# Performance work log

Measured on AMD Instinct MI355X. Metric: run time of the kernel, lower is better.

## Reference

```python
import jax, jax.numpy as jnp
import numpy as np

N_EMBD = 768
N_HEADS = 12

def setup_inputs() -> dict:
    key = jax.random.key(0)
    ks = jax.random.split(key, 5)
    B, T, C = 8, 1024, N_EMBD
    s_in = 1.0 / np.sqrt(C)
    x = jax.random.normal(ks[0], (B, T, C), dtype=jnp.float32)
    W_attn = jax.random.normal(ks[1], (C, 3 * C), dtype=jnp.float32) * s_in
    b_attn = jnp.zeros((3 * C,), dtype=jnp.float32)
    W_proj = jax.random.normal(ks[2], (C, C), dtype=jnp.float32) * s_in
    b_proj = jnp.zeros((C,), dtype=jnp.float32)
    return {"x": x, "W_attn": W_attn, "b_attn": b_attn, "W_proj": W_proj, "b_proj": b_proj}

def reference(x, W_attn, b_attn, W_proj, b_proj):
    B, T, C = x.shape
    H = N_HEADS
    hd = C // H
    qkv = x @ W_attn + b_attn                      # [B,T,3C]
    q, k, v = jnp.split(qkv, 3, axis=-1)
    # [B,T,C] -> [B,H,T,hd]
    q = q.reshape(B, T, H, hd).transpose(0, 2, 1, 3)
    k = k.reshape(B, T, H, hd).transpose(0, 2, 1, 3)
    v = v.reshape(B, T, H, hd).transpose(0, 2, 1, 3)
    att = jnp.einsum('bhqd,bhkd->bhqk', q, k) * (1.0 / np.sqrt(hd))
    mask = jnp.tril(jnp.ones((T, T), dtype=bool))
    att = jnp.where(mask, att, -jnp.inf)
    att = jax.nn.softmax(att, axis=-1)
    y = jnp.einsum('bhqk,bhkd->bhqd', att, v)      # [B,H,T,hd]
    y = y.transpose(0, 2, 1, 3).reshape(B, T, C)
    return y @ W_proj + b_proj
```

## Files before the change

### kernel.cpp

```cpp
#include <hip/hip_runtime.h>
#include <hip/hip_bf16.h>
#include <cmath>

typedef __bf16 bf16_t;
typedef __bf16 bf16x8 __attribute__((ext_vector_type(8)));
typedef float f32x4 __attribute__((ext_vector_type(4)));

#define MFMA16(A, B, C) __builtin_amdgcn_mfma_f32_16x16x32_bf16(A, B, C, 0, 0, 0)

#define GLOAD_LDS16(g, l)                                                      \
  __builtin_amdgcn_global_load_lds(                                            \
      (const __attribute__((address_space(1))) void*)(g),                      \
      (__attribute__((address_space(3))) void*)(l), 16, 0, 0)

__global__ __launch_bounds__(256) void f32_to_bf16(
    const float* __restrict__ src, bf16_t* __restrict__ dst) {
  const size_t i = (size_t)blockIdx.x * 256 + threadIdx.x;
  const float4 a0 = ((const float4*)src)[i * 2];
  const float4 a1 = ((const float4*)src)[i * 2 + 1];
  bf16x8 v = {(bf16_t)a0.x, (bf16_t)a0.y, (bf16_t)a0.z, (bf16_t)a0.w,
              (bf16_t)a1.x, (bf16_t)a1.y, (bf16_t)a1.z, (bf16_t)a1.w};
  ((bf16x8*)dst)[i] = v;
}

__global__ __launch_bounds__(256) void transpose_f32_to_bf16(
    const float* __restrict__ src, bf16_t* __restrict__ dst, int R, int C) {
  __shared__ bf16_t tile[32][33];
  const int c0 = blockIdx.x * 32, r0 = blockIdx.y * 32;
  const int tr = threadIdx.x >> 5;
  const int tc = threadIdx.x & 31;
#pragma unroll
  for (int i = 0; i < 32; i += 8)
    tile[tr + i][tc] = (bf16_t)src[(size_t)(r0 + tr + i) * C + (c0 + tc)];
  __syncthreads();
#pragma unroll
  for (int i = 0; i < 32; i += 8)
    dst[(size_t)(c0 + tr + i) * R + (r0 + tc)] = tile[tc][tr + i];
}

__global__ __launch_bounds__(768, 1) void gemm_qkv(
    const bf16_t* __restrict__ A, const bf16_t* __restrict__ BT,
    const float* __restrict__ bias,
    bf16_t* __restrict__ o0, bf16_t* __restrict__ o1, bf16_t* __restrict__ o2,
    int K) {
  extern __shared__ __align__(16) bf16_t smem[];
  constexpr int ASZ = 256 * 64;
  constexpr int BSZ = 288 * 64;
  bf16_t* Bbase = smem + 2 * ASZ;

  const int tid = threadIdx.x;
  const int w = tid >> 6, lane = tid & 63;
  const int wr = w / 6, wc = w % 6;
  const int quad = lane >> 4, l16 = lane & 15;

  const int id = blockIdx.x;
  const int xcd = id & 7;
  const int lin = id >> 3;
  const int nt = lin & 7;
  const int mt = (xcd << 2) + (lin >> 3);

  const int dr = lane >> 3;
  const int dc = (((lane & 7) - dr) & 7) << 3;

  const int so0 = ((quad + (l16 & 7)) & 7) << 3;
  const int so1 = so0 ^ 32;

  f32x4 acc[8][3] = {};

  auto stage = [&](int t, int s) {
    const size_t ko = (size_t)t * 64 + dc;
#pragma unroll
    for (int j = 0; j < 6; ++j) {
      const int u = w + j * 12;
      if (u < 32) {
        GLOAD_LDS16(A + (size_t)(mt * 256 + u * 8 + dr) * K + ko,
                    smem + s * ASZ + u * 8 * 64);
      } else if (u < 68) {
        const int v = u - 32;
        GLOAD_LDS16(BT + (size_t)(nt * 288 + v * 8 + dr) * K + ko,
                    Bbase + s * BSZ + v * 8 * 64);
      }
    }
  };

  auto compute = [&](int s) {
#pragma unroll
    for (int ks = 0; ks < 2; ++ks) {
      const int so = ks ? so1 : so0;
      bf16x8 bfrag[3], afrag[8];
#pragma unroll
      for (int ni = 0; ni < 3; ++ni)
        bfrag[ni] = *(const bf16x8*)(Bbase + s * BSZ +
                                     (wc * 48 + ni * 16 + l16) * 64 + so);
#pragma unroll
      for (int mi = 0; mi < 8; ++mi)
        afrag[mi] = *(const bf16x8*)(smem + s * ASZ +
                                     (wr * 128 + mi * 16 + l16) * 64 + so);
      __builtin_amdgcn_s_setprio(1);
#pragma unroll
      for (int mi = 0; mi < 8; ++mi)
#pragma unroll
        for (int ni = 0; ni < 3; ++ni)
          acc[mi][ni] = MFMA16(afrag[mi], bfrag[ni], acc[mi][ni]);
      __builtin_amdgcn_s_setprio(0);
    }
  };

  const int NIT = K / 64;
  stage(0, 0);
  __syncthreads();
  for (int t = 0; t < NIT; ++t) {
    if (t + 1 < NIT) stage(t + 1, (t + 1) & 1);
    compute(t & 1);
    if (t + 1 < NIT) __syncthreads();
  }

  const int m_base = mt * 256 + wr * 128;
  const int n_base = nt * 288 + wc * 48;
#pragma unroll
  for (int ni = 0; ni < 3; ++ni) {
    const int n = n_base + ni * 16 + l16;
    const float bv = bias[n];
    const int which = n / 768;
    const int c = n - which * 768;
    const int h = c >> 6, d = c & 63;
#pragma unroll
    for (int mi = 0; mi < 8; ++mi) {
#pragma unroll
      for (int r = 0; r < 4; ++r) {
        const int m = m_base + mi * 16 + quad * 4 + r;
        const bf16_t bw = (bf16_t)(acc[mi][ni][r] + bv);
        const int b = m >> 10, t = m & 1023;
        const size_t bh = (size_t)(b * 12 + h);
        if (which == 0)
          o0[(bh * 1024 + t) * 64 + d] = bw;
        else if (which == 1)
          o1[(bh * 1024 + t) * 64 + d] = bw;
        else
          o2[(bh * 64 + d) * 1024 + t] = bw;
      }
    }
  }
}

__global__ __launch_bounds__(256) void gemm_proj(
    const bf16_t* __restrict__ A, const bf16_t* __restrict__ BT,
    const float* __restrict__ bias, float* __restrict__ of, int N, int K) {
  constexpr int BM = 128, BN = 128, BK = 32;
  __shared__ __align__(16) bf16_t As[2][BM][BK];
  __shared__ __align__(16) bf16_t Bs[2][BN][BK];

  const int tid = threadIdx.x;
  const int wave = tid >> 6, lane = tid & 63;
  const int wr = wave >> 1, wc = wave & 1;
  const int quad = lane >> 4, l16 = lane & 15;

  const int id = blockIdx.x;
  const int xcd = id & 7;
  const int lin = id >> 3;
  const int nt = lin % 6;
  const int mt = xcd * 8 + lin / 6;

  const int rl = lane >> 2;
  const int cq = ((lane & 3) - (rl >> 1)) & 3;
  const int ac = cq << 3;
  const bf16_t* Ag0 = A + (size_t)(mt * BM + wave * 32 + rl) * K + ac;
  const bf16_t* Ag1 = Ag0 + (size_t)16 * K;
  const bf16_t* Bg0 = BT + (size_t)(nt * BN + wave * 32 + rl) * K + ac;
  const bf16_t* Bg1 = Bg0 + (size_t)16 * K;

  const int sw = ((quad + (l16 >> 1)) & 3) << 3;

  f32x4 acc[4][4] = {};

  auto stage = [&](int k0, int buf) {
    GLOAD_LDS16(Ag0 + k0, &As[buf][wave * 32][0]);
    GLOAD_LDS16(Ag1 + k0, &As[buf][wave * 32 + 16][0]);
    GLOAD_LDS16(Bg0 + k0, &Bs[buf][wave * 32][0]);
    GLOAD_LDS16(Bg1 + k0, &Bs[buf][wave * 32 + 16][0]);
  };
  auto compute = [&](int buf) {
    bf16x8 af[4], bfr[4];
#pragma unroll
    for (int mi = 0; mi < 4; ++mi)
      af[mi] = *(const bf16x8*)(&As[buf][wr * 64 + mi * 16 + l16][sw]);
#pragma unroll
    for (int ni = 0; ni < 4; ++ni)
      bfr[ni] = *(const bf16x8*)(&Bs[buf][wc * 64 + ni * 16 + l16][sw]);
#pragma unroll
    for (int mi = 0; mi < 4; ++mi)
#pragma unroll
      for (int ni = 0; ni < 4; ++ni)
        acc[mi][ni] = MFMA16(af[mi], bfr[ni], acc[mi][ni]);
  };

  const int NIT = K / BK;
  stage(0, 0);
  for (int k = 0; k + 2 < NIT; k += 2) {
    __syncthreads();
    stage((k + 1) * BK, 1);
    compute(0);
    __syncthreads();
    stage((k + 2) * BK, 0);
    compute(1);
  }
  __syncthreads();
  stage((NIT - 1) * BK, 1);
  compute(0);
  __syncthreads();
  compute(1);

  const int m_base = mt * BM + wr * 64;
  const int n_base = nt * BN + wc * 64;
#pragma unroll
  for (int ni = 0; ni < 4; ++ni) {
    const int n = n_base + ni * 16 + l16;
    const float bv = bias[n];
#pragma unroll
    for (int mi = 0; mi < 4; ++mi)
#pragma unroll
      for (int r = 0; r < 4; ++r) {
        const int m = m_base + mi * 16 + quad * 4 + r;
        of[(size_t)m * N + n] = acc[mi][ni][r] + bv;
      }
  }
}

__global__ __launch_bounds__(256) void attn_fwd(
    const bf16_t* __restrict__ Q, const bf16_t* __restrict__ Kg,
    const bf16_t* __restrict__ VT, bf16_t* __restrict__ Y) {
  __shared__ __align__(16) bf16_t Ks[2][64][64];
  __shared__ __align__(16) bf16_t Vs[2][64][64];
  __shared__ __align__(16) bf16_t Ps[4][16][72];

  const int tid = threadIdx.x;
  const int w = tid >> 6, lane = tid & 63;
  const int quad = lane >> 4, l16 = lane & 15;

  const int id = blockIdx.x;
  const int xcd = id & 7;
  const int lin = id >> 3;
  const int pair = lin & 7;
  const int h = lin >> 3;
  const int b = xcd;
  const size_t bh = (size_t)(b * 12 + h);
  const bf16_t* Qbh = Q + bh * 65536;
  const bf16_t* Kbh = Kg + bh * 65536;
  const bf16_t* VTbh = VT + bh * 65536;

  const int drow = lane >> 3;
  const int dchunk = (((lane & 7) - drow) & 7) << 3;

  const int so0 = ((quad + (l16 & 7)) & 7) << 3;
  const int so1 = so0 ^ 32;

  constexpr float SC = 0.18033688011112042f;
  constexpr float FM = 12.0f;
  const bf16_t one_b = (bf16_t)1.0f;
  const bf16x8 ones = {one_b, one_b, one_b, one_b,
                       one_b, one_b, one_b, one_b};

  auto stageKV = [&](int kt, int bufi) {
#pragma unroll
    for (int j = 0; j < 2; ++j) {
      const int r = w * 16 + j * 8 + drow;
      GLOAD_LDS16(Kbh + (size_t)(kt * 64 + r) * 64 + dchunk,
                  &Ks[bufi][w * 16 + j * 8][0]);
      GLOAD_LDS16(VTbh + (size_t)r * 1024 + kt * 64 + dchunk,
                  &Vs[bufi][w * 16 + j * 8][0]);
    }
  };

  for (int phase = 0; phase < 2; ++phase) {
    const int qt = phase ? pair : (15 - pair);

    const int qrow = qt * 64 + w * 16 + l16;
    bf16x8 qf0 = *(const bf16x8*)(Qbh + (size_t)qrow * 64 + quad * 8);
    bf16x8 qf1 = *(const bf16x8*)(Qbh + (size_t)qrow * 64 + 32 + quad * 8);

    f32x4 o[5] = {};

    __syncthreads();
    stageKV(0, 0);
    int buf = 0;
    for (int kt = 0; kt <= qt; ++kt) {
      __syncthreads();
      if (kt < qt) stageKV(kt + 1, buf ^ 1);

      f32x4 s[4];
#pragma unroll
      for (int ni = 0; ni < 4; ++ni) {
        bf16x8 kf0 = *(const bf16x8*)(&Ks[buf][ni * 16 + l16][so0]);
        bf16x8 kf1 = *(const bf16x8*)(&Ks[buf][ni * 16 + l16][so1]);
        f32x4 t = {};
        t = MFMA16(qf0, kf0, t);
        t = MFMA16(qf1, kf1, t);
        s[ni] = t;
      }
      if (kt == qt) {
#pragma unroll
        for (int ni = 0; ni < 4; ++ni)
#pragma unroll
          for (int r = 0; r < 4; ++r) {
            const int kp = ni * 16 + l16;
            const int qr = w * 16 + quad * 4 + r;
            const float p =
                (kp > qr) ? 0.0f : exp2f(fmaf(s[ni][r], SC, -FM));
            Ps[w][quad * 4 + r][ni * 16 + l16] = (bf16_t)p;
          }
      } else {
#pragma unroll
        for (int ni = 0; ni < 4; ++ni)
#pragma unroll
          for (int r = 0; r < 4; ++r)
            Ps[w][quad * 4 + r][ni * 16 + l16] =
                (bf16_t)exp2f(fmaf(s[ni][r], SC, -FM));
      }

      bf16x8 pf0 = *(const bf16x8*)(&Ps[w][l16][quad * 8]);
      bf16x8 pf1 = *(const bf16x8*)(&Ps[w][l16][32 + quad * 8]);
#pragma unroll
      for (int nd = 0; nd < 4; ++nd) {
        bf16x8 vf0 = *(const bf16x8*)(&Vs[buf][nd * 16 + l16][so0]);
        bf16x8 vf1 = *(const bf16x8*)(&Vs[buf][nd * 16 + l16][so1]);
        o[nd] = MFMA16(pf0, vf0, o[nd]);
        o[nd] = MFMA16(pf1, vf1, o[nd]);
      }
      o[4] = MFMA16(pf0, ones, o[4]);
      o[4] = MFMA16(pf1, ones, o[4]);
      buf ^= 1;
    }

#pragma unroll
    for (int r = 0; r < 4; ++r) {
      const float inv = 1.0f / o[4][r];
      const int t = qt * 64 + w * 16 + quad * 4 + r;
      bf16_t* yrow = Y + ((size_t)b * 1024 + t) * 768 + h * 64;
#pragma unroll
      for (int nd = 0; nd < 4; ++nd)
        yrow[nd * 16 + l16] = (bf16_t)(o[nd][r] * inv);
    }
  }
}

extern "C" void kernel_launch(void* const* d_in, const int* in_sizes, int n_in,
                              void* d_out, int out_size, void* d_ws,
                              size_t ws_size, hipStream_t stream) {
  const float* x      = (const float*)d_in[0];
  const float* W_attn = (const float*)d_in[1];
  const float* b_attn = (const float*)d_in[2];
  const float* W_proj = (const float*)d_in[3];
  const float* b_proj = (const float*)d_in[4];
  float* out = (float*)d_out;

  const size_t HEADS = 96;
  bf16_t* wta = (bf16_t*)d_ws;
  bf16_t* wtp = wta + (size_t)2304 * 768;
  bf16_t* qw  = wtp + (size_t)768 * 768;
  bf16_t* kw  = qw + HEADS * 1024 * 64;
  bf16_t* vtw = kw + HEADS * 1024 * 64;
  bf16_t* yw  = vtw + HEADS * 1024 * 64;
  bf16_t* xb  = yw + (size_t)8192 * 768;

  f32_to_bf16<<<dim3(8192 * 768 / (256 * 8)), 256, 0, stream>>>(x, xb);
  transpose_f32_to_bf16<<<dim3(2304 / 32, 768 / 32), 256, 0, stream>>>(
      W_attn, wta, 768, 2304);
  transpose_f32_to_bf16<<<dim3(768 / 32, 768 / 32), 256, 0, stream>>>(
      W_proj, wtp, 768, 768);
  const size_t qkv_lds = (size_t)(2 * (256 + 288) * 64) * sizeof(bf16_t);
  gemm_qkv<<<dim3(256), 768, qkv_lds, stream>>>(
      xb, wta, b_attn, qw, kw, vtw, 768);
  attn_fwd<<<dim3(768), 256, 0, stream>>>(qw, kw, vtw, yw);
  gemm_proj<<<dim3(384), 256, 0, stream>>>(
      yw, wtp, b_proj, out, 768, 768);
}
```

Baseline: 200.2 us.

## Share K/V tile loads between paired causal query tiles in attention

```diff
diff --git a/kernel.cpp b/kernel.cpp
--- a/kernel.cpp
+++ b/kernel.cpp
@@ -226,7 +226,7 @@
   }
 }
 
-__global__ __launch_bounds__(256) void attn_fwd(
+__global__ __launch_bounds__(256, 3) void attn_fwd(
     const bf16_t* __restrict__ Q, const bf16_t* __restrict__ Kg,
     const bf16_t* __restrict__ VT, bf16_t* __restrict__ Y) {
   __shared__ __align__(16) bf16_t Ks[2][64][64];
@@ -271,75 +271,86 @@
     }
   };
 
-  for (int phase = 0; phase < 2; ++phase) {
-    const int qt = phase ? pair : (15 - pair);
-
-    const int qrow = qt * 64 + w * 16 + l16;
-    bf16x8 qf0 = *(const bf16x8*)(Qbh + (size_t)qrow * 64 + quad * 8);
-    bf16x8 qf1 = *(const bf16x8*)(Qbh + (size_t)qrow * 64 + 32 + quad * 8);
-
-    f32x4 o[5] = {};
-
+  const int qtb = 15 - pair;
+  const int qts = pair;
+
+  const int qrb = qtb * 64 + w * 16 + l16;
+  const int qrs = qts * 64 + w * 16 + l16;
+  const bf16x8 qb0 = *(const bf16x8*)(Qbh + (size_t)qrb * 64 + quad * 8);
+  const bf16x8 qb1 = *(const bf16x8*)(Qbh + (size_t)qrb * 64 + 32 + quad * 8);
+  const bf16x8 qs0 = *(const bf16x8*)(Qbh + (size_t)qrs * 64 + quad * 8);
+  const bf16x8 qs1 = *(const bf16x8*)(Qbh + (size_t)qrs * 64 + 32 + quad * 8);
+
+  f32x4 ob[5] = {};
+  f32x4 os[5] = {};
+
+  auto compute_q = [&](f32x4* o, const bf16x8& q0, const bf16x8& q1,
+                       int bufi, bool diag) {
+    f32x4 s[4];
+#pragma unroll
+    for (int ni = 0; ni < 4; ++ni) {
+      bf16x8 kf0 = *(const bf16x8*)(&Ks[bufi][ni * 16 + l16][so0]);
+      bf16x8 kf1 = *(const bf16x8*)(&Ks[bufi][ni * 16 + l16][so1]);
+      f32x4 t = {};
+      t = MFMA16(q0, kf0, t);
+      t = MFMA16(q1, kf1, t);
+      s[ni] = t;
+    }
+    if (diag) {
+#pragma unroll
+      for (int ni = 0; ni < 4; ++ni)
+#pragma unroll
+        for (int r = 0; r < 4; ++r) {
+          const int kp = ni * 16 + l16;
+          const int qr = w * 16 + quad * 4 + r;
+          const float p = (kp > qr) ? 0.0f : exp2f(fmaf(s[ni][r], SC, -FM));
+          Ps[w][quad * 4 + r][ni * 16 + l16] = (bf16_t)p;
+        }
+    } else {
+#pragma unroll
+      for (int ni = 0; ni < 4; ++ni)
+#pragma unroll
+        for (int r = 0; r < 4; ++r)
+          Ps[w][quad * 4 + r][ni * 16 + l16] =
+              (bf16_t)exp2f(fmaf(s[ni][r], SC, -FM));
+    }
+    bf16x8 pf0 = *(const bf16x8*)(&Ps[w][l16][quad * 8]);
+    bf16x8 pf1 = *(const bf16x8*)(&Ps[w][l16][32 + quad * 8]);
+#pragma unroll
+    for (int nd = 0; nd < 4; ++nd) {
+      bf16x8 vf0 = *(const bf16x8*)(&Vs[bufi][nd * 16 + l16][so0]);
+      bf16x8 vf1 = *(const bf16x8*)(&Vs[bufi][nd * 16 + l16][so1]);
+      o[nd] = MFMA16(pf0, vf0, o[nd]);
+      o[nd] = MFMA16(pf1, vf1, o[nd]);
+    }
+    o[4] = MFMA16(pf0, ones, o[4]);
+    o[4] = MFMA16(pf1, ones, o[4]);
+  };
+
+  stageKV(0, 0);
+  int buf = 0;
+  for (int kt = 0; kt <= qtb; ++kt) {
     __syncthreads();
-    stageKV(0, 0);
-    int buf = 0;
-    for (int kt = 0; kt <= qt; ++kt) {
-      __syncthreads();
-      if (kt < qt) stageKV(kt + 1, buf ^ 1);
-
-      f32x4 s[4];
-#pragma unroll
-      for (int ni = 0; ni < 4; ++ni) {
-        bf16x8 kf0 = *(const bf16x8*)(&Ks[buf][ni * 16 + l16][so0]);
-        bf16x8 kf1 = *(const bf16x8*)(&Ks[buf][ni * 16 + l16][so1]);
-        f32x4 t = {};
-        t = MFMA16(qf0, kf0, t);
-        t = MFMA16(qf1, kf1, t);
-        s[ni] = t;
-      }
-      if (kt == qt) {
-#pragma unroll
-        for (int ni = 0; ni < 4; ++ni)
-#pragma unroll
-          for (int r = 0; r < 4; ++r) {
-            const int kp = ni * 16 + l16;
-            const int qr = w * 16 + quad * 4 + r;
-            const float p =
-                (kp > qr) ? 0.0f : exp2f(fmaf(s[ni][r], SC, -FM));
-            Ps[w][quad * 4 + r][ni * 16 + l16] = (bf16_t)p;
-          }
-      } else {
-#pragma unroll
-        for (int ni = 0; ni < 4; ++ni)
-#pragma unroll
-          for (int r = 0; r < 4; ++r)
-            Ps[w][quad * 4 + r][ni * 16 + l16] =
-                (bf16_t)exp2f(fmaf(s[ni][r], SC, -FM));
-      }
-
-      bf16x8 pf0 = *(const bf16x8*)(&Ps[w][l16][quad * 8]);
-      bf16x8 pf1 = *(const bf16x8*)(&Ps[w][l16][32 + quad * 8]);
-#pragma unroll
-      for (int nd = 0; nd < 4; ++nd) {
-        bf16x8 vf0 = *(const bf16x8*)(&Vs[buf][nd * 16 + l16][so0]);
-        bf16x8 vf1 = *(const bf16x8*)(&Vs[buf][nd * 16 + l16][so1]);
-        o[nd] = MFMA16(pf0, vf0, o[nd]);
-        o[nd] = MFMA16(pf1, vf1, o[nd]);
-      }
-      o[4] = MFMA16(pf0, ones, o[4]);
-      o[4] = MFMA16(pf1, ones, o[4]);
-      buf ^= 1;
-    }
-
-#pragma unroll
-    for (int r = 0; r < 4; ++r) {
-      const float inv = 1.0f / o[4][r];
-      const int t = qt * 64 + w * 16 + quad * 4 + r;
-      bf16_t* yrow = Y + ((size_t)b * 1024 + t) * 768 + h * 64;
-#pragma unroll
-      for (int nd = 0; nd < 4; ++nd)
-        yrow[nd * 16 + l16] = (bf16_t)(o[nd][r] * inv);
-    }
+    if (kt < qtb) stageKV(kt + 1, buf ^ 1);
+    compute_q(ob, qb0, qb1, buf, kt == qtb);
+    if (kt <= qts) compute_q(os, qs0, qs1, buf, kt == qts);
+    buf ^= 1;
+  }
+
+#pragma unroll
+  for (int r = 0; r < 4; ++r) {
+    const float invb = 1.0f / ob[4][r];
+    const int tb = qtb * 64 + w * 16 + quad * 4 + r;
+    bf16_t* yb = Y + ((size_t)b * 1024 + tb) * 768 + h * 64;
+#pragma unroll
+    for (int nd = 0; nd < 4; ++nd)
+      yb[nd * 16 + l16] = (bf16_t)(ob[nd][r] * invb);
+    const float invs = 1.0f / os[4][r];
+    const int ts = qts * 64 + w * 16 + quad * 4 + r;
+    bf16_t* ys = Y + ((size_t)b * 1024 + ts) * 768 + h * 64;
+#pragma unroll
+    for (int nd = 0; nd < 4; ++nd)
+      ys[nd * 16 + l16] = (bf16_t)(os[nd][r] * invs);
   }
 }
 
```

Measured after the change: 198.7 us. Within noise of the previous version (-0.7%).
